# Kernel tuning notes

Hardware: AMD Instinct MI355X
Metric: run time of the kernel (lower is better)

## Reference

```python
import jax, jax.numpy as jnp
import numpy as np

ROPE_BASE = 10000.0

def _rope(x, positions):
    # x: (B, h, T, d); standard half-split rotary embedding with d_key = d
    d = x.shape[-1]
    inv_freq = 1.0 / (ROPE_BASE ** (jnp.arange(0, d // 2, dtype=jnp.float32) / (d // 2)))
    ang = positions.astype(jnp.float32)[:, None] * inv_freq[None, :]  # (T, d/2)
    cos, sin = jnp.cos(ang), jnp.sin(ang)
    x1, x2 = x[..., : d // 2], x[..., d // 2 :]
    return jnp.concatenate([x1 * cos - x2 * sin, x1 * sin + x2 * cos], axis=-1)


def setup_inputs() -> dict:
    key = jax.random.key(0)
    k1, k2, k3 = jax.random.split(key, 3)
    B, T, d, h = 2, 2048, 768, 8
    std = d ** -0.5
    x = jax.random.normal(k1, (B, T, d), dtype=jnp.float32)
    M = jax.random.normal(k2, (d, h * d), dtype=jnp.float32) * std
    V = jax.random.normal(k3, (d, h * d), dtype=jnp.float32) * std
    positions = jnp.arange(T, dtype=jnp.int32)
    return {"x": x, "M": M, "V": V, "positions": positions}


def reference(x, M, V, positions):
    B, T, d = x.shape
    h = M.shape[1] // d
    scale = 1.0 / jnp.sqrt(jnp.float32(d))
    # Q = RoPE(X @ M), K = RoPE(X) broadcast across heads, val = X @ V
    Q = (x @ M).reshape(B, T, h, d).transpose(0, 2, 1, 3)   # (B,h,T,d)
    val = (x @ V).reshape(B, T, h, d).transpose(0, 2, 1, 3)  # (B,h,T,d)
    K = jnp.broadcast_to(x[:, None, :, :], (B, h, T, d))     # (B,h,T,d)
    Q = _rope(Q, positions)
    K = _rope(K, positions)
    scores = jnp.einsum("bhqd,bhkd->bhqk", Q, K) * scale     # (B,h,T,T)
    causal = jnp.tril(jnp.ones((T, T), dtype=bool))          # True = keep
    scores = jnp.where(causal[None, None], scores, -jnp.inf)
    attn = jax.nn.softmax(scores, axis=-1)
    out = jnp.einsum("bhqk,bhkd->bhqd", attn, val)
    return out.sum(axis=1)  # sum over heads -> (B,T,d)
```

## Files before the change

kernel.cpp:

```cpp
#include <hip/hip_runtime.h>
#include <hip/hip_bf16.h>

typedef __bf16 bf16x8 __attribute__((ext_vector_type(8)));
typedef float f32x4 __attribute__((ext_vector_type(4)));
typedef float f32x16 __attribute__((ext_vector_type(16)));

#define SCALE 0.03608439182435161f
#define NEGINF (-1e30f)

static __device__ __forceinline__ ushort f2bf(float f) {
    union { float f; unsigned u; } v; v.f = f;
    unsigned r = (v.u + 0x7fff + ((v.u >> 16) & 1)) >> 16;
    return (ushort)r;
}
static __device__ __forceinline__ float bf2f(ushort u) {
    union { unsigned u; float f; } v; v.u = ((unsigned)u) << 16;
    return v.f;
}

static __device__ __forceinline__ void gload16(const void* g, void* lds) {
    __builtin_amdgcn_global_load_lds((const __attribute__((address_space(1))) void*)g,
                                     (__attribute__((address_space(3))) void*)lds, 16, 0, 0);
}

#define PHASE_SYNC do { asm volatile("s_waitcnt vmcnt(0) lgkmcnt(0)" ::: "memory"); \
                        __builtin_amdgcn_s_barrier(); \
                        asm volatile("" ::: "memory"); } while (0)
#define BARL do { asm volatile("s_waitcnt lgkmcnt(0)" ::: "memory"); \
                  __builtin_amdgcn_s_barrier(); \
                  asm volatile("" ::: "memory"); } while (0)

__global__ void k_convx(const float* __restrict__ x, ushort* __restrict__ xb, int n4) {
    int i = blockIdx.x * blockDim.x + threadIdx.x;
    if (i >= n4) return;
    float4 v = ((const float4*)x)[i];
    ushort4 o; o.x = f2bf(v.x); o.y = f2bf(v.y); o.z = f2bf(v.z); o.w = f2bf(v.w);
    ((ushort4*)xb)[i] = o;
}

__global__ void k_tconv(const float* __restrict__ in, ushort* __restrict__ out, int R, int C) {
    __shared__ float ts[32][33];
    int r0 = blockIdx.x * 32, c0 = blockIdx.y * 32;
    int lr = threadIdx.x >> 5, lc = threadIdx.x & 31;
#pragma unroll
    for (int i = 0; i < 4; i++) ts[lr + i * 8][lc] = in[(r0 + lr + i * 8) * C + c0 + lc];
    __syncthreads();
#pragma unroll
    for (int i = 0; i < 4; i++) out[(c0 + lr + i * 8) * R + r0 + lc] = f2bf(ts[lc][lr + i * 8]);
}

template <int EPI>
__global__ __launch_bounds__(256) void k_gemm(const ushort* __restrict__ A,
                                              const ushort* __restrict__ Bt,
                                              ushort* __restrict__ out) {
    __shared__ ushort As[128 * 40];
    __shared__ ushort Bs[128 * 40];
    const int m0 = blockIdx.x * 128, n0 = blockIdx.y * 128;
    const int tid = threadIdx.x, lane = tid & 63, wid = tid >> 6;
    const int wm = (wid >> 1) * 64, wn = (wid & 1) * 64;
    f32x4 acc[4][4] = {};

    for (int kt = 0; kt < 768; kt += 32) {
#pragma unroll
        for (int i = 0; i < 2; i++) {
            int c = tid + i * 256;
            int row = c >> 2, kc = (c & 3) * 8;
            uint4 va = *(const uint4*)&A[(m0 + row) * 768 + kt + kc];
            *(uint4*)&As[row * 40 + kc] = va;
            uint4 vb = *(const uint4*)&Bt[(n0 + row) * 768 + kt + kc];
            *(uint4*)&Bs[row * 40 + kc] = vb;
        }
        __syncthreads();
        bf16x8 af[4], bfr[4];
#pragma unroll
        for (int m = 0; m < 4; m++)
            af[m] = *(const bf16x8*)&As[(wm + m * 16 + (lane & 15)) * 40 + (lane >> 4) * 8];
#pragma unroll
        for (int n = 0; n < 4; n++)
            bfr[n] = *(const bf16x8*)&Bs[(wn + n * 16 + (lane & 15)) * 40 + (lane >> 4) * 8];
#pragma unroll
        for (int m = 0; m < 4; m++)
#pragma unroll
            for (int n = 0; n < 4; n++)
                acc[m][n] = __builtin_amdgcn_mfma_f32_16x16x32_bf16(af[m], bfr[n], acc[m][n], 0, 0, 0);
        __syncthreads();
    }

#pragma unroll
    for (int m = 0; m < 4; m++) {
#pragma unroll
        for (int n = 0; n < 4; n++) {
#pragma unroll
            for (int r = 0; r < 4; r++) {
                int row = m0 + wm + m * 16 + (lane >> 4) * 4 + r;
                int col = n0 + wn + n * 16 + (lane & 15);
                float v = acc[m][n][r];
                int idx;
                if (EPI == 0) {
                    int b = row >> 11, t = row & 2047;
                    int hh = col / 768, dd = col - hh * 768;
                    idx = ((b * 8 + hh) * 2048 + t) * 768 + dd;
                } else {
                    int hh = row / 768, dd = row - hh * 768;
                    int b = col >> 11, t = col & 2047;
                    idx = ((b * 8 + hh) * 768 + dd) * 2048 + t;
                }
                out[idx] = f2bf(v);
            }
        }
    }
}

__global__ void k_ropeq(ushort* __restrict__ Q, const int* __restrict__ pos, int nrows) {
    int i = blockIdx.x * blockDim.x + threadIdx.x;
    int row = i / 96, j4 = (i % 96) * 4;
    if (row >= nrows) return;
    float p = (float)pos[row & 2047];
    ushort4 u1 = *(ushort4*)&Q[row * 768 + j4];
    ushort4 u2 = *(ushort4*)&Q[row * 768 + 384 + j4];
    ushort4 o1, o2;
#pragma unroll
    for (int k = 0; k < 4; k++) {
        float inv = exp2f(-(float)(j4 + k) * (13.287712379549449f / 384.0f));
        float ang = p * inv;
        float s, c; sincosf(ang, &s, &c);
        float x1 = bf2f(((ushort*)&u1)[k]), x2 = bf2f(((ushort*)&u2)[k]);
        ((ushort*)&o1)[k] = f2bf((x1 * c - x2 * s) * SCALE);
        ((ushort*)&o2)[k] = f2bf((x1 * s + x2 * c) * SCALE);
    }
    *(ushort4*)&Q[row * 768 + j4] = o1;
    *(ushort4*)&Q[row * 768 + 384 + j4] = o2;
}

__global__ void k_ropek(const float* __restrict__ x, ushort* __restrict__ Kr,
                        const int* __restrict__ pos, int nrows) {
    int i = blockIdx.x * blockDim.x + threadIdx.x;
    int row = i / 96, j4 = (i % 96) * 4;
    if (row >= nrows) return;
    float p = (float)pos[row & 2047];
    float4 x1 = *(const float4*)&x[row * 768 + j4];
    float4 x2 = *(const float4*)&x[row * 768 + 384 + j4];
    ushort4 o1, o2;
    float a1[4] = {x1.x, x1.y, x1.z, x1.w};
    float a2[4] = {x2.x, x2.y, x2.z, x2.w};
#pragma unroll
    for (int k = 0; k < 4; k++) {
        float inv = exp2f(-(float)(j4 + k) * (13.287712379549449f / 384.0f));
        float ang = p * inv;
        float s, c; sincosf(ang, &s, &c);
        ((ushort*)&o1)[k] = f2bf(a1[k] * c - a2[k] * s);
        ((ushort*)&o2)[k] = f2bf(a1[k] * s + a2[k] * c);
    }
    *(ushort4*)&Kr[row * 768 + j4] = o1;
    *(ushort4*)&Kr[row * 768 + 384 + j4] = o2;
}

__global__ __launch_bounds__(512, 2) void k_attn(const ushort* Qr, const ushort* __restrict__ Kr,
                                                 const ushort* __restrict__ valT, ushort* Oh) {
    __shared__ alignas(128) char Qs[98304];
    __shared__ alignas(128) char pool[65536];

    const int p = blockIdx.x, hh = blockIdx.y, b = blockIdx.z;
    const int bh = b * 8 + hh;
    const int tid = threadIdx.x, lane = tid & 63, wid = tid >> 6;
    const int g = wid & 3, qh = wid >> 2;
    const int l31 = lane & 31, hi = lane >> 5;
    const int hi16 = hi << 4;

    const int row0 = tid >> 4, col16 = tid & 15;
    const int swz = (col16 << 4) ^ ((row0 & 15) << 4);

    const int arow = g * 32 + l31;
    const int qrow = qh * 32 + l31;
    const int asw = (arow & 15) << 4;
    const int qsw = (qrow & 15) << 4;

    char* Pb = pool + 32768;
    float* pmax_s = (float*)(pool + 49152);
    float* psum_s = (float*)(pool + 50176);
    float* stat_s = (float*)(pool + 51200);

    const char* Kb0 = (const char*)Kr + ((size_t)(b * 2048 + row0)) * 1536 + swz;
    const char* Vb0 = (const char*)valT + ((size_t)(bh * 768 + row0)) * 4096 + swz;

    for (int ti = 0; ti < 2; ti++) {
        const int qt = ti ? (31 - p) : p;
        const int q0 = qt * 64;
        const int nkb = (qt + 2) >> 1;
        const int qg = q0 + qrow;

        const char* qsrc = (const char*)Qr + ((size_t)(bh * 2048 + q0 + row0)) * 1536 + swz;
#pragma unroll
        for (int r = 0; r < 12; r++)
            gload16(qsrc + (r >> 1) * 256 + (size_t)(r & 1) * 49152,
                    Qs + (r >> 1) * 16384 + (r & 1) * 8192 + wid * 1024);
#pragma unroll
        for (int r = 0; r < 4; r++)
            gload16(Kb0 + (size_t)r * 49152, pool + r * 8192 + wid * 1024);

        float m_r = NEGINF, l_r = 0.f;
        f32x16 oacc[6] = {};

        for (int kb = 0; kb < nkb; kb++) {
            const char* kc = Kb0 + (size_t)kb * 196608;
            const char* vc = Vb0 + (size_t)kb * 256;

            f32x16 sacc = {};
#pragma unroll
            for (int c = 0; c < 6; c++) {
                PHASE_SYNC;
                if (c < 5) {
#pragma unroll
                    for (int r = 0; r < 4; r++)
                        gload16(kc + (c + 1) * 256 + (size_t)r * 49152,
                                pool + ((c + 1) & 1) * 32768 + r * 8192 + wid * 1024);
                } else {
#pragma unroll
                    for (int r = 0; r < 4; r++)
                        gload16(vc + (size_t)r * 131072, pool + r * 8192 + wid * 1024);
                }
                const char* kbuf = pool + (c & 1) * 32768;
                const char* qcb = Qs + c * 16384;
                __builtin_amdgcn_s_setprio(1);
#pragma unroll
                for (int s = 0; s < 8; s++) {
                    bf16x8 a = *(const bf16x8*)(kbuf + arow * 256 + ((s * 32 + hi16) ^ asw));
                    bf16x8 bq = *(const bf16x8*)(qcb + qrow * 256 + ((s * 32 + hi16) ^ qsw));
                    sacc = __builtin_amdgcn_mfma_f32_32x32x16_bf16(a, bq, sacc, 0, 0, 0);
                }
                __builtin_amdgcn_s_setprio(0);
            }

            __builtin_amdgcn_s_barrier();

            const int kbase_ = kb * 128 + g * 32 + 4 * hi;
            float mloc = NEGINF;
#pragma unroll
            for (int r = 0; r < 16; r++) {
                int kg = kbase_ + (r & 3) + 8 * (r >> 2);
                float v = (kg > qg) ? NEGINF : sacc[r];
                mloc = fmaxf(mloc, v);
            }
            mloc = fmaxf(mloc, __shfl_xor(mloc, 32));
            if (hi == 0) pmax_s[qrow * 4 + g] = mloc;
            BARL;

            float4 pm = *(const float4*)&pmax_s[qrow * 4];
            float m_new = fmaxf(fmaxf(fmaxf(pm.x, pm.y), fmaxf(pm.z, pm.w)), m_r);
            float rv = __expf(m_r - m_new);
            float ps = 0.f; uint w[8];
#pragma unroll
            for (int j = 0; j < 8; j++) {
                int kg0 = kbase_ + ((2 * j) & 3) + 8 * ((2 * j) >> 2);
                int kg1 = kbase_ + ((2 * j + 1) & 3) + 8 * ((2 * j + 1) >> 2);
                float e0 = (kg0 > qg) ? 0.f : __expf(sacc[2 * j] - m_new);
                float e1 = (kg1 > qg) ? 0.f : __expf(sacc[2 * j + 1] - m_new);
                ps += e0 + e1;
                w[j] = (uint)f2bf(e0) | ((uint)f2bf(e1) << 16);
            }
            ps += __shfl_xor(ps, 32);
            if (hi == 0) psum_s[qrow * 4 + g] = ps;
            if (g == 0 && hi == 0) stat_s[qrow] = rv;
#pragma unroll
            for (int j = 0; j < 4; j++) {
                uint2 pw; pw.x = w[2 * j]; pw.y = w[2 * j + 1];
                *(uint2*)(Pb + qrow * 256 + ((g * 64 + j * 16 + hi * 8) ^ qsw)) = pw;
            }
            BARL;

            float4 ps4 = *(const float4*)&psum_s[qrow * 4];
            l_r = l_r * rv + (ps4.x + ps4.y + ps4.z + ps4.w);
            m_r = m_new;
            float rs[16];
#pragma unroll
            for (int r = 0; r < 16; r++)
                rs[r] = stat_s[qh * 32 + (r & 3) + 8 * (r >> 2) + 4 * hi];
#pragma unroll
            for (int c = 0; c < 6; c++)
#pragma unroll
                for (int r = 0; r < 16; r++) oacc[c][r] *= rs[r];
            bf16x8 pa[8];
#pragma unroll
            for (int s = 0; s < 8; s++)
                pa[s] = *(const bf16x8*)(Pb + qrow * 256 + ((s * 32 + hi16) ^ qsw));

#pragma unroll
            for (int c = 0; c < 6; c++) {
                PHASE_SYNC;
                if (c < 5) {
#pragma unroll
                    for (int r = 0; r < 4; r++)
                        gload16(vc + (size_t)(c + 1) * 524288 + (size_t)r * 131072,
                                pool + ((c + 1) & 1) * 32768 + r * 8192 + wid * 1024);
                } else if (kb + 1 < nkb) {
#pragma unroll
                    for (int r = 0; r < 4; r++)
                        gload16(kc + 196608 + (size_t)r * 49152, pool + r * 8192 + wid * 1024);
                }
                const char* vbuf = pool + (c & 1) * 32768;
                __builtin_amdgcn_s_setprio(1);
#pragma unroll
                for (int s = 0; s < 8; s++) {
                    bf16x8 bv = *(const bf16x8*)(vbuf + arow * 256 + ((s * 32 + hi16) ^ asw));
                    oacc[c] = __builtin_amdgcn_mfma_f32_32x32x16_bf16(pa[s], bv, oacc[c], 0, 0, 0);
                }
                __builtin_amdgcn_s_setprio(0);
            }
        }

        asm volatile("s_waitcnt vmcnt(0) lgkmcnt(0)" ::: "memory");
        __builtin_amdgcn_s_barrier();
        if (g == 0 && hi == 0) stat_s[qrow] = l_r;
        BARL;
        float inv16[16];
#pragma unroll
        for (int r = 0; r < 16; r++)
            inv16[r] = 1.0f / stat_s[qh * 32 + (r & 3) + 8 * (r >> 2) + 4 * hi];
        BARL;
        ushort* obase = Oh + ((size_t)(bh * 2048 + q0 + qh * 32)) * 768;
#pragma unroll
        for (int c = 0; c < 6; c++) {
            int dd = c * 128 + g * 32 + l31;
#pragma unroll
            for (int r = 0; r < 16; r++) {
                int rq = (r & 3) + 8 * (r >> 2) + 4 * hi;
                obase[(size_t)rq * 768 + dd] = f2bf(oacc[c][r] * inv16[r]);
            }
        }
    }
}

__global__ void k_reduce(const ushort* __restrict__ Oh, float* __restrict__ out) {
    int i = blockIdx.x * blockDim.x + threadIdx.x;
    if (i >= 786432) return;
    size_t base = (size_t)i * 4;
    int b = (base >= 1572864) ? 1 : 0;
    size_t rem = base - (size_t)b * 1572864;
    const ushort* src = Oh + (size_t)b * 8 * 1572864 + rem;
    float4 acc = {0.f, 0.f, 0.f, 0.f};
#pragma unroll
    for (int h = 0; h < 8; h++) {
        ushort4 v = *(const ushort4*)(src + (size_t)h * 1572864);
        acc.x += bf2f(v.x); acc.y += bf2f(v.y); acc.z += bf2f(v.z); acc.w += bf2f(v.w);
    }
    *(float4*)&out[base] = acc;
}

extern "C" void kernel_launch(void* const* d_in, const int* in_sizes, int n_in,
                              void* d_out, int out_size, void* d_ws, size_t ws_size,
                              hipStream_t stream) {
    const float* x = (const float*)d_in[0];
    const float* M = (const float*)d_in[1];
    const float* V = (const float*)d_in[2];
    const int* pos = (const int*)d_in[3];
    float* out = (float*)d_out;
    char* ws = (char*)d_ws;

    ushort* xb   = (ushort*)(ws);
    ushort* Mt   = (ushort*)(ws + 6291456);
    ushort* Vt   = (ushort*)(ws + 15728640);
    ushort* Qr   = (ushort*)(ws + 25165824);
    ushort* valT = (ushort*)(ws + 75497472);
    ushort* Kr   = (ushort*)(ws + 125829120);

    k_convx<<<3072, 256, 0, stream>>>(x, xb, 786432);
    k_tconv<<<dim3(24, 192), 256, 0, stream>>>(M, Mt, 768, 6144);
    k_tconv<<<dim3(24, 192), 256, 0, stream>>>(V, Vt, 768, 6144);
    k_gemm<0><<<dim3(32, 48), 256, 0, stream>>>(xb, Mt, Qr);
    k_gemm<1><<<dim3(48, 32), 256, 0, stream>>>(Vt, xb, valT);
    k_ropeq<<<12288, 256, 0, stream>>>(Qr, pos, 32768);
    k_ropek<<<1536, 256, 0, stream>>>(x, Kr, pos, 4096);
    k_attn<<<dim3(16, 8, 2), 512, 0, stream>>>(Qr, Kr, valT, Qr );
    k_reduce<<<3072, 256, 0, stream>>>(Qr, out);
}
```

Measured before the change: 371.6 us.

## Deepen K/V global-to-LDS prefetch to two stages with partial vmcnt waits

Restructures the double-buffered K and V chunk loads so each buffer is refilled two chunks ahead, issued after the MFMA block finishes reading it. Waits now use vmcnt(4) instead of draining all outstanding loads, so one chunk's transfer stays in flight while the current chunk is computed. This is meant to hide global load latency that previously stalled each phase at a full vmcnt(0) barrier. The cost is an extra barrier per chunk and more delicate ordering of buffer reuse; a wrong vmcnt count or buffer index could cause races.

After: 371.4 us. Within noise of the previous version (-0.1%).

```diff
diff --git a/kernel.cpp b/kernel.cpp
--- a/kernel.cpp
+++ b/kernel.cpp
@@ -23,6 +23,9 @@
                                      (__attribute__((address_space(3))) void*)lds, 16, 0, 0);
 }
 
+#define WAITVM4 asm volatile("s_waitcnt vmcnt(4)" ::: "memory")
+#define WAITVM0 asm volatile("s_waitcnt vmcnt(0)" ::: "memory")
+#define BARX __builtin_amdgcn_s_barrier()
 #define PHASE_SYNC do { asm volatile("s_waitcnt vmcnt(0) lgkmcnt(0)" ::: "memory"); \
                         __builtin_amdgcn_s_barrier(); \
                         asm volatile("" ::: "memory"); } while (0)
@@ -197,6 +200,9 @@
 #pragma unroll
         for (int r = 0; r < 4; r++)
             gload16(Kb0 + (size_t)r * 49152, pool + r * 8192 + wid * 1024);
+#pragma unroll
+        for (int r = 0; r < 4; r++)
+            gload16(Kb0 + 256 + (size_t)r * 49152, pool + 32768 + r * 8192 + wid * 1024);
 
         float m_r = NEGINF, l_r = 0.f;
         f32x16 oacc[6] = {};
@@ -204,21 +210,12 @@
         for (int kb = 0; kb < nkb; kb++) {
             const char* kc = Kb0 + (size_t)kb * 196608;
             const char* vc = Vb0 + (size_t)kb * 256;
+            const bool nx = (kb + 1 < nkb);
 
             f32x16 sacc = {};
 #pragma unroll
             for (int c = 0; c < 6; c++) {
-                PHASE_SYNC;
-                if (c < 5) {
-#pragma unroll
-                    for (int r = 0; r < 4; r++)
-                        gload16(kc + (c + 1) * 256 + (size_t)r * 49152,
-                                pool + ((c + 1) & 1) * 32768 + r * 8192 + wid * 1024);
-                } else {
-#pragma unroll
-                    for (int r = 0; r < 4; r++)
-                        gload16(vc + (size_t)r * 131072, pool + r * 8192 + wid * 1024);
-                }
+                WAITVM4; BARX;
                 const char* kbuf = pool + (c & 1) * 32768;
                 const char* qcb = Qs + c * 16384;
                 __builtin_amdgcn_s_setprio(1);
@@ -229,9 +226,18 @@
                     sacc = __builtin_amdgcn_mfma_f32_32x32x16_bf16(a, bq, sacc, 0, 0, 0);
                 }
                 __builtin_amdgcn_s_setprio(0);
-            }
-
-            __builtin_amdgcn_s_barrier();
+                BARX;
+                if (c < 4) {
+#pragma unroll
+                    for (int r = 0; r < 4; r++)
+                        gload16(kc + (c + 2) * 256 + (size_t)r * 49152,
+                                pool + (c & 1) * 32768 + r * 8192 + wid * 1024);
+                } else if (c == 4) {
+#pragma unroll
+                    for (int r = 0; r < 4; r++)
+                        gload16(vc + (size_t)r * 131072, pool + r * 8192 + wid * 1024);
+                }
+            }
 
             const int kbase_ = kb * 128 + g * 32 + 4 * hi;
             float mloc = NEGINF;
@@ -286,16 +292,16 @@
 
 #pragma unroll
             for (int c = 0; c < 6; c++) {
-                PHASE_SYNC;
-                if (c < 5) {
-#pragma unroll
-                    for (int r = 0; r < 4; r++)
-                        gload16(vc + (size_t)(c + 1) * 524288 + (size_t)r * 131072,
-                                pool + ((c + 1) & 1) * 32768 + r * 8192 + wid * 1024);
-                } else if (kb + 1 < nkb) {
-#pragma unroll
-                    for (int r = 0; r < 4; r++)
-                        gload16(kc + 196608 + (size_t)r * 49152, pool + r * 8192 + wid * 1024);
+                if (c == 0) {
+                    PHASE_SYNC;
+#pragma unroll
+                    for (int r = 0; r < 4; r++)
+                        gload16(vc + 524288 + (size_t)r * 131072,
+                                pool + 32768 + r * 8192 + wid * 1024);
+                } else if (c < 5 || nx) {
+                    WAITVM4; BARX;
+                } else {
+                    WAITVM0; BARX;
                 }
                 const char* vbuf = pool + (c & 1) * 32768;
                 __builtin_amdgcn_s_setprio(1);
@@ -305,11 +311,30 @@
                     oacc[c] = __builtin_amdgcn_mfma_f32_32x32x16_bf16(pa[s], bv, oacc[c], 0, 0, 0);
                 }
                 __builtin_amdgcn_s_setprio(0);
+                BARX;
+                if (c == 0) {
+#pragma unroll
+                    for (int r = 0; r < 4; r++)
+                        gload16(vc + 2 * 524288 + (size_t)r * 131072,
+                                pool + r * 8192 + wid * 1024);
+                } else if (c < 4) {
+#pragma unroll
+                    for (int r = 0; r < 4; r++)
+                        gload16(vc + (size_t)(c + 2) * 524288 + (size_t)r * 131072,
+                                pool + (c & 1) * 32768 + r * 8192 + wid * 1024);
+                } else if (c == 4 && nx) {
+#pragma unroll
+                    for (int r = 0; r < 4; r++)
+                        gload16(kc + 196608 + (size_t)r * 49152, pool + r * 8192 + wid * 1024);
+                } else if (c == 5 && nx) {
+#pragma unroll
+                    for (int r = 0; r < 4; r++)
+                        gload16(kc + 196608 + 256 + (size_t)r * 49152,
+                                pool + 32768 + r * 8192 + wid * 1024);
+                }
             }
         }
 
-        asm volatile("s_waitcnt vmcnt(0) lgkmcnt(0)" ::: "memory");
-        __builtin_amdgcn_s_barrier();
         if (g == 0 && hi == 0) stat_s[qrow] = l_r;
         BARL;
         float inv16[16];
```

## Pre-swizzle K and V into MFMA fragment layout and load directly to registers

Applied to the files above, without the earlier changes.

The K-rope kernel and the value GEMM epilogue now write K and V in a fragment-major layout that matches the MFMA operand order. The attention kernel then loads K/V fragments straight from global memory into registers with a double-buffered register prefetch, instead of staging them through LDS. This removes the per-chunk LDS staging, the waitcnt+barrier phase syncs, and the LDS reads for K/V, and frees 64KB of shared memory. In exchange it raises register pressure and relies on global/L2 latency being hidden by the software prefetch. Each wave also reads K/V redundantly from global memory where it previously shared them through LDS.

Measured after the change: 527.1 us. +41.9%, slower.

```diff
diff --git a/kernel.cpp b/kernel.cpp
--- a/kernel.cpp
+++ b/kernel.cpp
@@ -23,9 +23,6 @@
                                      (__attribute__((address_space(3))) void*)lds, 16, 0, 0);
 }
 
-#define PHASE_SYNC do { asm volatile("s_waitcnt vmcnt(0) lgkmcnt(0)" ::: "memory"); \
-                        __builtin_amdgcn_s_barrier(); \
-                        asm volatile("" ::: "memory"); } while (0)
 #define BARL do { asm volatile("s_waitcnt lgkmcnt(0)" ::: "memory"); \
                   __builtin_amdgcn_s_barrier(); \
                   asm volatile("" ::: "memory"); } while (0)
@@ -95,17 +92,17 @@
                 int row = m0 + wm + m * 16 + (lane >> 4) * 4 + r;
                 int col = n0 + wn + n * 16 + (lane & 15);
                 float v = acc[m][n][r];
-                int idx;
                 if (EPI == 0) {
                     int b = row >> 11, t = row & 2047;
                     int hh = col / 768, dd = col - hh * 768;
-                    idx = ((b * 8 + hh) * 2048 + t) * 768 + dd;
+                    out[((b * 8 + hh) * 2048 + t) * 768 + dd] = f2bf(v);
                 } else {
                     int hh = row / 768, dd = row - hh * 768;
                     int b = col >> 11, t = col & 2047;
-                    idx = ((b * 8 + hh) * 768 + dd) * 2048 + t;
-                }
-                out[idx] = f2bf(v);
+                    size_t unit = (((((size_t)(b * 8 + hh) * 16 + (t >> 7)) * 6 + (dd >> 7)) * 8
+                                    + ((t >> 4) & 7)) * 2 + ((t >> 3) & 1)) * 128 + (dd & 127);
+                    out[unit * 8 + (t & 7)] = f2bf(v);
+                }
             }
         }
     }
@@ -132,33 +129,48 @@
     *(ushort4*)&Q[row * 768 + 384 + j4] = o2;
 }
 
-__global__ void k_ropek(const float* __restrict__ x, ushort* __restrict__ Kr,
-                        const int* __restrict__ pos, int nrows) {
+__global__ void k_ropekf(const float* __restrict__ x, char* __restrict__ Kf,
+                         const int* __restrict__ pos) {
     int i = blockIdx.x * blockDim.x + threadIdx.x;
-    int row = i / 96, j4 = (i % 96) * 4;
-    if (row >= nrows) return;
-    float p = (float)pos[row & 2047];
-    float4 x1 = *(const float4*)&x[row * 768 + j4];
-    float4 x2 = *(const float4*)&x[row * 768 + 384 + j4];
-    ushort4 o1, o2;
-    float a1[4] = {x1.x, x1.y, x1.z, x1.w};
-    float a2[4] = {x2.x, x2.y, x2.z, x2.w};
-#pragma unroll
-    for (int k = 0; k < 4; k++) {
-        float inv = exp2f(-(float)(j4 + k) * (13.287712379549449f / 384.0f));
+    if (i >= 393216) return;
+    int row = i / 96, d8 = i - row * 96;
+    int t = row & 2047, b = row >> 11;
+    float p = (float)pos[t];
+    int d = d8 * 8;
+    bool lo = d < 384;
+    int j0 = lo ? d : d - 384;
+    float4 xa = *(const float4*)&x[row * 768 + j0];
+    float4 xc = *(const float4*)&x[row * 768 + j0 + 4];
+    float4 ya = *(const float4*)&x[row * 768 + j0 + 384];
+    float4 yc = *(const float4*)&x[row * 768 + j0 + 388];
+    float x1[8] = {xa.x, xa.y, xa.z, xa.w, xc.x, xc.y, xc.z, xc.w};
+    float x2[8] = {ya.x, ya.y, ya.z, ya.w, yc.x, yc.y, yc.z, yc.w};
+    ushort o[8];
+#pragma unroll
+    for (int k = 0; k < 8; k++) {
+        float inv = exp2f(-(float)(j0 + k) * (13.287712379549449f / 384.0f));
         float ang = p * inv;
         float s, c; sincosf(ang, &s, &c);
-        ((ushort*)&o1)[k] = f2bf(a1[k] * c - a2[k] * s);
-        ((ushort*)&o2)[k] = f2bf(a1[k] * s + a2[k] * c);
-    }
-    *(ushort4*)&Kr[row * 768 + j4] = o1;
-    *(ushort4*)&Kr[row * 768 + 384 + j4] = o2;
-}
-
-__global__ __launch_bounds__(512, 2) void k_attn(const ushort* Qr, const ushort* __restrict__ Kr,
-                                                 const ushort* __restrict__ valT, ushort* Oh) {
+        o[k] = f2bf(lo ? x1[k] * c - x2[k] * s : x1[k] * s + x2[k] * c);
+    }
+    int kb = t >> 7, r = t & 127;
+    int c2 = d8 >> 4, rem = d8 & 15, s2 = rem >> 1, hi = rem & 1;
+    size_t unit = ((((size_t)(b * 16 + kb) * 6 + c2) * 8 + s2) * 2 + hi) * 128 + r;
+    uint4 w;
+    w.x = o[0] | ((uint)o[1] << 16); w.y = o[2] | ((uint)o[3] << 16);
+    w.z = o[4] | ((uint)o[5] << 16); w.w = o[6] | ((uint)o[7] << 16);
+    *(uint4*)(Kf + unit * 16) = w;
+}
+
+__global__ __launch_bounds__(512, 2) void k_attn(const ushort* Qr,
+                                                 const char* __restrict__ Kf,
+                                                 const char* __restrict__ Vf,
+                                                 ushort* Oh) {
     __shared__ alignas(128) char Qs[98304];
-    __shared__ alignas(128) char pool[65536];
+    __shared__ alignas(128) char Pb[16384];
+    __shared__ float pmax_s[256];
+    __shared__ float psum_s[256];
+    __shared__ float stat_s[64];
 
     const int p = blockIdx.x, hh = blockIdx.y, b = blockIdx.z;
     const int bh = b * 8 + hh;
@@ -170,18 +182,11 @@
     const int row0 = tid >> 4, col16 = tid & 15;
     const int swz = (col16 << 4) ^ ((row0 & 15) << 4);
 
-    const int arow = g * 32 + l31;
     const int qrow = qh * 32 + l31;
-    const int asw = (arow & 15) << 4;
     const int qsw = (qrow & 15) << 4;
 
-    char* Pb = pool + 32768;
-    float* pmax_s = (float*)(pool + 49152);
-    float* psum_s = (float*)(pool + 50176);
-    float* stat_s = (float*)(pool + 51200);
-
-    const char* Kb0 = (const char*)Kr + ((size_t)(b * 2048 + row0)) * 1536 + swz;
-    const char* Vb0 = (const char*)valT + ((size_t)(bh * 768 + row0)) * 4096 + swz;
+    const char* kfl = Kf + (size_t)b * 3145728 + (size_t)(hi * 128 + g * 32 + l31) * 16;
+    const char* vfl = Vf + (size_t)bh * 3145728 + (size_t)(hi * 128 + g * 32 + l31) * 16;
 
     for (int ti = 0; ti < 2; ti++) {
         const int qt = ti ? (31 - p) : p;
@@ -194,44 +199,47 @@
         for (int r = 0; r < 12; r++)
             gload16(qsrc + (r >> 1) * 256 + (size_t)(r & 1) * 49152,
                     Qs + (r >> 1) * 16384 + (r & 1) * 8192 + wid * 1024);
-#pragma unroll
-        for (int r = 0; r < 4; r++)
-            gload16(Kb0 + (size_t)r * 49152, pool + r * 8192 + wid * 1024);
+
+        bf16x8 kf0[8], kf1[8];
+#pragma unroll
+        for (int s = 0; s < 8; s++)
+            kf0[s] = *(const bf16x8*)(kfl + s * 4096);
+
+        asm volatile("s_waitcnt vmcnt(0)" ::: "memory");
+        __builtin_amdgcn_s_barrier();
 
         float m_r = NEGINF, l_r = 0.f;
         f32x16 oacc[6] = {};
 
         for (int kb = 0; kb < nkb; kb++) {
-            const char* kc = Kb0 + (size_t)kb * 196608;
-            const char* vc = Vb0 + (size_t)kb * 256;
-
+            const char* kcb = kfl + (size_t)kb * 196608;
+            const char* vcb = vfl + (size_t)kb * 196608;
+            const bool nx = (kb + 1 < nkb);
+
+            bf16x8 vf0[8], vf1[8];
             f32x16 sacc = {};
+
 #pragma unroll
             for (int c = 0; c < 6; c++) {
-                PHASE_SYNC;
                 if (c < 5) {
 #pragma unroll
-                    for (int r = 0; r < 4; r++)
-                        gload16(kc + (c + 1) * 256 + (size_t)r * 49152,
-                                pool + ((c + 1) & 1) * 32768 + r * 8192 + wid * 1024);
+                    for (int s = 0; s < 8; s++) {
+                        bf16x8 v = *(const bf16x8*)(kcb + (c + 1) * 32768 + s * 4096);
+                        if ((c & 1) == 0) kf1[s] = v; else kf0[s] = v;
+                    }
                 } else {
 #pragma unroll
-                    for (int r = 0; r < 4; r++)
-                        gload16(vc + (size_t)r * 131072, pool + r * 8192 + wid * 1024);
-                }
-                const char* kbuf = pool + (c & 1) * 32768;
-                const char* qcb = Qs + c * 16384;
+                    for (int s = 0; s < 8; s++)
+                        vf0[s] = *(const bf16x8*)(vcb + s * 4096);
+                }
                 __builtin_amdgcn_s_setprio(1);
 #pragma unroll
                 for (int s = 0; s < 8; s++) {
-                    bf16x8 a = *(const bf16x8*)(kbuf + arow * 256 + ((s * 32 + hi16) ^ asw));
-                    bf16x8 bq = *(const bf16x8*)(qcb + qrow * 256 + ((s * 32 + hi16) ^ qsw));
-                    sacc = __builtin_amdgcn_mfma_f32_32x32x16_bf16(a, bq, sacc, 0, 0, 0);
+                    bf16x8 bq = *(const bf16x8*)(Qs + c * 16384 + qrow * 256 + ((s * 32 + hi16) ^ qsw));
+                    sacc = __builtin_amdgcn_mfma_f32_32x32x16_bf16((c & 1) ? kf1[s] : kf0[s], bq, sacc, 0, 0, 0);
                 }
                 __builtin_amdgcn_s_setprio(0);
             }
-
-            __builtin_amdgcn_s_barrier();
 
             const int kbase_ = kb * 128 + g * 32 + 4 * hi;
             float mloc = NEGINF;
@@ -286,37 +294,33 @@
 
 #pragma unroll
             for (int c = 0; c < 6; c++) {
-                PHASE_SYNC;
                 if (c < 5) {
 #pragma unroll
-                    for (int r = 0; r < 4; r++)
-                        gload16(vc + (size_t)(c + 1) * 524288 + (size_t)r * 131072,
-                                pool + ((c + 1) & 1) * 32768 + r * 8192 + wid * 1024);
-                } else if (kb + 1 < nkb) {
-#pragma unroll
-                    for (int r = 0; r < 4; r++)
-                        gload16(kc + 196608 + (size_t)r * 49152, pool + r * 8192 + wid * 1024);
-                }
-                const char* vbuf = pool + (c & 1) * 32768;
+                    for (int s = 0; s < 8; s++) {
+                        bf16x8 v = *(const bf16x8*)(vcb + (c + 1) * 32768 + s * 4096);
+                        if ((c & 1) == 0) vf1[s] = v; else vf0[s] = v;
+                    }
+                }
+                if (c == 2 && nx) {
+#pragma unroll
+                    for (int s = 0; s < 8; s++)
+                        kf0[s] = *(const bf16x8*)(kcb + 196608 + s * 4096);
+                }
                 __builtin_amdgcn_s_setprio(1);
 #pragma unroll
-                for (int s = 0; s < 8; s++) {
-                    bf16x8 bv = *(const bf16x8*)(vbuf + arow * 256 + ((s * 32 + hi16) ^ asw));
-                    oacc[c] = __builtin_amdgcn_mfma_f32_32x32x16_bf16(pa[s], bv, oacc[c], 0, 0, 0);
-                }
+                for (int s = 0; s < 8; s++)
+                    oacc[c] = __builtin_amdgcn_mfma_f32_32x32x16_bf16(pa[s], (c & 1) ? vf1[s] : vf0[s], oacc[c], 0, 0, 0);
                 __builtin_amdgcn_s_setprio(0);
             }
         }
 
-        asm volatile("s_waitcnt vmcnt(0) lgkmcnt(0)" ::: "memory");
-        __builtin_amdgcn_s_barrier();
+        BARL;
         if (g == 0 && hi == 0) stat_s[qrow] = l_r;
         BARL;
         float inv16[16];
 #pragma unroll
         for (int r = 0; r < 16; r++)
             inv16[r] = 1.0f / stat_s[qh * 32 + (r & 3) + 8 * (r >> 2) + 4 * hi];
-        BARL;
         ushort* obase = Oh + ((size_t)(bh * 2048 + q0 + qh * 32)) * 768;
 #pragma unroll
         for (int c = 0; c < 6; c++) {
@@ -356,20 +360,20 @@
     float* out = (float*)d_out;
     char* ws = (char*)d_ws;
 
-    ushort* xb   = (ushort*)(ws);
-    ushort* Mt   = (ushort*)(ws + 6291456);
-    ushort* Vt   = (ushort*)(ws + 15728640);
-    ushort* Qr   = (ushort*)(ws + 25165824);
-    ushort* valT = (ushort*)(ws + 75497472);
-    ushort* Kr   = (ushort*)(ws + 125829120);
+    ushort* xb = (ushort*)(ws);
+    ushort* Mt = (ushort*)(ws + 6291456);
+    ushort* Vt = (ushort*)(ws + 15728640);
+    ushort* Qr = (ushort*)(ws + 25165824);
+    ushort* Vf = (ushort*)(ws + 75497472);
+    char*   Kf = (char*)(ws + 125829120);
 
     k_convx<<<3072, 256, 0, stream>>>(x, xb, 786432);
     k_tconv<<<dim3(24, 192), 256, 0, stream>>>(M, Mt, 768, 6144);
     k_tconv<<<dim3(24, 192), 256, 0, stream>>>(V, Vt, 768, 6144);
     k_gemm<0><<<dim3(32, 48), 256, 0, stream>>>(xb, Mt, Qr);
-    k_gemm<1><<<dim3(48, 32), 256, 0, stream>>>(Vt, xb, valT);
+    k_gemm<1><<<dim3(48, 32), 256, 0, stream>>>(Vt, xb, Vf);
     k_ropeq<<<12288, 256, 0, stream>>>(Qr, pos, 32768);
-    k_ropek<<<1536, 256, 0, stream>>>(x, Kr, pos, 4096);
-    k_attn<<<dim3(16, 8, 2), 512, 0, stream>>>(Qr, Kr, valT, Qr );
+    k_ropekf<<<1536, 256, 0, stream>>>(x, Kf, pos);
+    k_attn<<<dim3(16, 8, 2), 512, 0, stream>>>(Qr, Kf, (const char*)Vf, Qr );
     k_reduce<<<3072, 256, 0, stream>>>(Qr, out);
 }
```

## Use direct global-to-LDS loads in GEMM and skip causal masking on unmasked tiles

Applied to the files above, without the earlier changes.

The projection GEMM now stages A and B tiles with global_load_lds directly into an unpadded LDS layout instead of going through registers into padded shared arrays. The barriers are replaced with explicit waitcnt-plus-barrier macros. In the attention kernel, key blocks that lie entirely below the diagonal skip the per-element causal comparisons in the max and exp steps. The unpadded 32-element LDS rows may cause bank conflicts on the fragment reads, and the GEMM loses overlap because each tile load is waited on before compute.

After: 359.7 us. 1.03x faster.

```diff
diff --git a/kernel.cpp b/kernel.cpp
--- a/kernel.cpp
+++ b/kernel.cpp
@@ -23,9 +23,9 @@
                                      (__attribute__((address_space(3))) void*)lds, 16, 0, 0);
 }
 
-#define PHASE_SYNC do { asm volatile("s_waitcnt vmcnt(0) lgkmcnt(0)" ::: "memory"); \
-                        __builtin_amdgcn_s_barrier(); \
-                        asm volatile("" ::: "memory"); } while (0)
+#define PHASEB do { asm volatile("s_waitcnt vmcnt(0) lgkmcnt(0)" ::: "memory"); \
+                    __builtin_amdgcn_s_barrier(); \
+                    asm volatile("" ::: "memory"); } while (0)
 #define BARL do { asm volatile("s_waitcnt lgkmcnt(0)" ::: "memory"); \
                   __builtin_amdgcn_s_barrier(); \
                   asm volatile("" ::: "memory"); } while (0)
@@ -53,37 +53,34 @@
 __global__ __launch_bounds__(256) void k_gemm(const ushort* __restrict__ A,
                                               const ushort* __restrict__ Bt,
                                               ushort* __restrict__ out) {
-    __shared__ ushort As[128 * 40];
-    __shared__ ushort Bs[128 * 40];
+    __shared__ ushort As[128 * 32];
+    __shared__ ushort Bs[128 * 32];
     const int m0 = blockIdx.x * 128, n0 = blockIdx.y * 128;
     const int tid = threadIdx.x, lane = tid & 63, wid = tid >> 6;
     const int wm = (wid >> 1) * 64, wn = (wid & 1) * 64;
+    const int l15 = lane & 15, l4 = lane >> 4;
+    const int srow = tid >> 2, scol = (tid & 3) * 8;
     f32x4 acc[4][4] = {};
 
     for (int kt = 0; kt < 768; kt += 32) {
-#pragma unroll
-        for (int i = 0; i < 2; i++) {
-            int c = tid + i * 256;
-            int row = c >> 2, kc = (c & 3) * 8;
-            uint4 va = *(const uint4*)&A[(m0 + row) * 768 + kt + kc];
-            *(uint4*)&As[row * 40 + kc] = va;
-            uint4 vb = *(const uint4*)&Bt[(n0 + row) * 768 + kt + kc];
-            *(uint4*)&Bs[row * 40 + kc] = vb;
-        }
-        __syncthreads();
+        gload16(&A[(size_t)(m0 + srow) * 768 + kt + scol],       (char*)As + wid * 1024);
+        gload16(&A[(size_t)(m0 + 64 + srow) * 768 + kt + scol],  (char*)As + 4096 + wid * 1024);
+        gload16(&Bt[(size_t)(n0 + srow) * 768 + kt + scol],      (char*)Bs + wid * 1024);
+        gload16(&Bt[(size_t)(n0 + 64 + srow) * 768 + kt + scol], (char*)Bs + 4096 + wid * 1024);
+        PHASEB;
         bf16x8 af[4], bfr[4];
 #pragma unroll
         for (int m = 0; m < 4; m++)
-            af[m] = *(const bf16x8*)&As[(wm + m * 16 + (lane & 15)) * 40 + (lane >> 4) * 8];
+            af[m] = *(const bf16x8*)&As[(wm + m * 16 + l15) * 32 + l4 * 8];
 #pragma unroll
         for (int n = 0; n < 4; n++)
-            bfr[n] = *(const bf16x8*)&Bs[(wn + n * 16 + (lane & 15)) * 40 + (lane >> 4) * 8];
+            bfr[n] = *(const bf16x8*)&Bs[(wn + n * 16 + l15) * 32 + l4 * 8];
 #pragma unroll
         for (int m = 0; m < 4; m++)
 #pragma unroll
             for (int n = 0; n < 4; n++)
                 acc[m][n] = __builtin_amdgcn_mfma_f32_16x16x32_bf16(af[m], bfr[n], acc[m][n], 0, 0, 0);
-        __syncthreads();
+        BARL;
     }
 
 #pragma unroll
@@ -204,11 +201,13 @@
         for (int kb = 0; kb < nkb; kb++) {
             const char* kc = Kb0 + (size_t)kb * 196608;
             const char* vc = Vb0 + (size_t)kb * 256;
+            const bool nx = (kb + 1 < nkb);
+            const bool nm = (kb * 128 + 127 > q0);
 
             f32x16 sacc = {};
 #pragma unroll
             for (int c = 0; c < 6; c++) {
-                PHASE_SYNC;
+                PHASEB;
                 if (c < 5) {
 #pragma unroll
                     for (int r = 0; r < 4; r++)
@@ -231,15 +230,20 @@
                 __builtin_amdgcn_s_setprio(0);
             }
 
-            __builtin_amdgcn_s_barrier();
+            BARL;
 
             const int kbase_ = kb * 128 + g * 32 + 4 * hi;
             float mloc = NEGINF;
-#pragma unroll
-            for (int r = 0; r < 16; r++) {
-                int kg = kbase_ + (r & 3) + 8 * (r >> 2);
-                float v = (kg > qg) ? NEGINF : sacc[r];
-                mloc = fmaxf(mloc, v);
+            if (nm) {
+#pragma unroll
+                for (int r = 0; r < 16; r++) {
+                    int kg = kbase_ + (r & 3) + 8 * (r >> 2);
+                    float v = (kg > qg) ? NEGINF : sacc[r];
+                    mloc = fmaxf(mloc, v);
+                }
+            } else {
+#pragma unroll
+                for (int r = 0; r < 16; r++) mloc = fmaxf(mloc, sacc[r]);
             }
             mloc = fmaxf(mloc, __shfl_xor(mloc, 32));
             if (hi == 0) pmax_s[qrow * 4 + g] = mloc;
@@ -249,14 +253,24 @@
             float m_new = fmaxf(fmaxf(fmaxf(pm.x, pm.y), fmaxf(pm.z, pm.w)), m_r);
             float rv = __expf(m_r - m_new);
             float ps = 0.f; uint w[8];
-#pragma unroll
-            for (int j = 0; j < 8; j++) {
-                int kg0 = kbase_ + ((2 * j) & 3) + 8 * ((2 * j) >> 2);
-                int kg1 = kbase_ + ((2 * j + 1) & 3) + 8 * ((2 * j + 1) >> 2);
-                float e0 = (kg0 > qg) ? 0.f : __expf(sacc[2 * j] - m_new);
-                float e1 = (kg1 > qg) ? 0.f : __expf(sacc[2 * j + 1] - m_new);
-                ps += e0 + e1;
-                w[j] = (uint)f2bf(e0) | ((uint)f2bf(e1) << 16);
+            if (nm) {
+#pragma unroll
+                for (int j = 0; j < 8; j++) {
+                    int kg0 = kbase_ + ((2 * j) & 3) + 8 * ((2 * j) >> 2);
+                    int kg1 = kbase_ + ((2 * j + 1) & 3) + 8 * ((2 * j + 1) >> 2);
+                    float e0 = (kg0 > qg) ? 0.f : __expf(sacc[2 * j] - m_new);
+                    float e1 = (kg1 > qg) ? 0.f : __expf(sacc[2 * j + 1] - m_new);
+                    ps += e0 + e1;
+                    w[j] = (uint)f2bf(e0) | ((uint)f2bf(e1) << 16);
+                }
+            } else {
+#pragma unroll
+                for (int j = 0; j < 8; j++) {
+                    float e0 = __expf(sacc[2 * j] - m_new);
+                    float e1 = __expf(sacc[2 * j + 1] - m_new);
+                    ps += e0 + e1;
+                    w[j] = (uint)f2bf(e0) | ((uint)f2bf(e1) << 16);
+                }
             }
             ps += __shfl_xor(ps, 32);
             if (hi == 0) psum_s[qrow * 4 + g] = ps;
@@ -286,13 +300,13 @@
 
 #pragma unroll
             for (int c = 0; c < 6; c++) {
-                PHASE_SYNC;
+                PHASEB;
                 if (c < 5) {
 #pragma unroll
                     for (int r = 0; r < 4; r++)
                         gload16(vc + (size_t)(c + 1) * 524288 + (size_t)r * 131072,
                                 pool + ((c + 1) & 1) * 32768 + r * 8192 + wid * 1024);
-                } else if (kb + 1 < nkb) {
+                } else if (nx) {
 #pragma unroll
                     for (int r = 0; r < 4; r++)
                         gload16(kc + 196608 + (size_t)r * 49152, pool + r * 8192 + wid * 1024);
@@ -308,8 +322,7 @@
             }
         }
 
-        asm volatile("s_waitcnt vmcnt(0) lgkmcnt(0)" ::: "memory");
-        __builtin_amdgcn_s_barrier();
+        BARL;
         if (g == 0 && hi == 0) stat_s[qrow] = l_r;
         BARL;
         float inv16[16];
```
